# Kernel tuning notes

Measured on AMD Instinct MI355X. Metric: run time of the kernel, lower is better.

Reference implementation:

```python
import jax, jax.numpy as jnp
import numpy as np

NUM_EXPERTS = 32
TOP_K = 4
HIDDEN = 2048
INTER = 768


def setup_inputs() -> dict:
    key = jax.random.key(0)
    k1, k2, k3, k4 = jax.random.split(key, 4)
    hidden_states = jax.random.normal(k1, (4, 512, HIDDEN), dtype=jnp.float32)
    gate = jax.random.normal(k2, (HIDDEN, NUM_EXPERTS), dtype=jnp.float32) * 0.02
    gate_up_proj = jax.random.normal(k3, (NUM_EXPERTS, HIDDEN, 2 * INTER), dtype=jnp.float32) * 0.02
    down_proj = jax.random.normal(k4, (NUM_EXPERTS, INTER, HIDDEN), dtype=jnp.float32) * 0.02
    return {"hidden_states": hidden_states, "gate": gate,
            "gate_up_proj": gate_up_proj, "down_proj": down_proj}


def reference(hidden_states, gate, gate_up_proj, down_proj):
    batch_size = hidden_states.shape[0]
    x = hidden_states.reshape(-1, HIDDEN)  # (T, D)
    num_tokens = x.shape[0]

    # Router
    router_logits = jnp.einsum('TD,DE->TE', x, gate)
    routing_weights = jax.nn.softmax(router_logits.astype(jnp.float32), axis=-1)
    top_k_weights, top_k_indices = jax.lax.top_k(routing_weights, TOP_K)
    top_k_weights = top_k_weights / top_k_weights.sum(axis=-1, keepdims=True)
    top_k_weights = top_k_weights.astype(x.dtype)

    # Scatter top-k weights into full (T, E) matrix
    router_weights = jnp.zeros((num_tokens, NUM_EXPERTS), dtype=x.dtype)
    token_indices = jnp.broadcast_to(jnp.arange(num_tokens)[:, None], top_k_indices.shape)
    router_weights = router_weights.at[token_indices, top_k_indices].set(top_k_weights)

    # Dense all-expert experts pass (faithful to original: computes every expert per token)
    gate_up = jnp.einsum('TD,EDF->TEF', x, gate_up_proj)  # (T, E, 2F)
    g, u = jnp.split(gate_up, 2, axis=-1)
    gated = u * jax.nn.silu(g)  # (T, E, F)
    next_states = jnp.einsum('TEF,EFD->TED', gated, down_proj)
    next_states = (next_states * router_weights[..., None]).sum(axis=1)  # (T, D)
    return next_states.reshape(batch_size, -1, HIDDEN)
```

## Files before the change

### kernel.cpp

```cpp
#include <hip/hip_runtime.h>

#define T_TOKENS 2048
#define HIDDEN   2048
#define NEXPERT  32
#define TOPK     4
#define INTER    768
#define NPAIRS   (T_TOKENS*TOPK)
#define BM       128
#define BK       32
#define MT_MAX   95
#define NT1      12
#define NT2      16

typedef short  bh8 __attribute__((ext_vector_type(8)));
typedef float  fx4 __attribute__((ext_vector_type(4)));
typedef unsigned short us4 __attribute__((ext_vector_type(4)));

__device__ __forceinline__ unsigned short f2bf(float f){
    unsigned int u = __float_as_uint(f);
    u += 0x7FFFu + ((u >> 16) & 1u);
    return (unsigned short)(u >> 16);
}
__device__ __forceinline__ bh8 pk8(float4 a, float4 b){
    bh8 r;
    r[0]=(short)f2bf(a.x); r[1]=(short)f2bf(a.y); r[2]=(short)f2bf(a.z); r[3]=(short)f2bf(a.w);
    r[4]=(short)f2bf(b.x); r[5]=(short)f2bf(b.y); r[6]=(short)f2bf(b.z); r[7]=(short)f2bf(b.w);
    return r;
}

__global__ void router_k(const float* __restrict__ x, const float* __restrict__ gate,
                         int* __restrict__ topk_id, float* __restrict__ topk_w,
                         int* __restrict__ counts){
    const int t = blockIdx.x;
    const int l = threadIdx.x;
    const float* xr = x + (size_t)t*HIDDEN;
    float acc[NEXPERT];
#pragma unroll
    for (int e=0;e<NEXPERT;e++) acc[e]=0.f;
    for (int d=l; d<HIDDEN; d+=64){
        float xv = xr[d];
        const float4* g4 = (const float4*)(gate + (size_t)d*NEXPERT);
#pragma unroll
        for (int i=0;i<8;i++){
            float4 g = g4[i];
            acc[i*4+0] += xv*g.x; acc[i*4+1] += xv*g.y;
            acc[i*4+2] += xv*g.z; acc[i*4+3] += xv*g.w;
        }
    }
#pragma unroll
    for (int e=0;e<NEXPERT;e++){
#pragma unroll
        for (int m=1;m<64;m<<=1) acc[e] += __shfl_xor(acc[e], m, 64);
    }
    int ids[TOPK]; float lv[TOPK];
#pragma unroll
    for (int k=0;k<TOPK;k++){
        float m=-1e30f; int mi=0;
#pragma unroll
        for (int e=0;e<NEXPERT;e++){ if (acc[e]>m){ m=acc[e]; mi=e; } }
        ids[k]=mi; lv[k]=m; acc[mi]=-1e30f;
    }
    float ex[TOPK]; float s=0.f;
#pragma unroll
    for (int k=0;k<TOPK;k++){ ex[k]=__expf(lv[k]-lv[0]); s+=ex[k]; }
    if (l==0){
        float inv = 1.f/s;
#pragma unroll
        for (int k=0;k<TOPK;k++){
            topk_id[t*TOPK+k]=ids[k];
            topk_w[t*TOPK+k]=ex[k]*inv;
            atomicAdd(&counts[ids[k]],1);
        }
    }
}

__global__ void sched_k(const int* __restrict__ counts, int* __restrict__ offs,
                        int* __restrict__ cursors, int* __restrict__ nmt,
                        int* __restrict__ te, int* __restrict__ tr0, int* __restrict__ trn){
    if (threadIdx.x==0 && blockIdx.x==0){
        int tot=0, nm=0;
        for (int e=0;e<NEXPERT;e++){
            int c = counts[e];
            offs[e]=tot; cursors[e]=tot;
            for (int s=0;s<c;s+=BM){
                te[nm]=e; tr0[nm]=tot+s; trn[nm]=(c-s)<BM?(c-s):BM; nm++;
            }
            tot+=c;
        }
        *nmt = nm;
    }
}

__global__ void scatter_k(const int* __restrict__ topk_id, const float* __restrict__ topk_w,
                          int* __restrict__ cursors, int* __restrict__ pair_tok,
                          float* __restrict__ pair_w){
    int g = blockIdx.x*256 + threadIdx.x;
    int e = topk_id[g];
    float w = topk_w[g];
    int pos = atomicAdd(&cursors[e],1);
    pair_tok[pos] = g>>2;
    pair_w[pos]  = w;
}

__global__ __launch_bounds__(256) void gemm1_k(
        const float* __restrict__ x, const float* __restrict__ gup,
        const int* __restrict__ nmt, const int* __restrict__ te,
        const int* __restrict__ tr0, const int* __restrict__ trn,
        const int* __restrict__ pair_tok, const float* __restrict__ pair_w,
        unsigned short* __restrict__ gated){
    __shared__ unsigned short As[BM*40];
    __shared__ unsigned short Bs[BM*40];
    __shared__ int   s_tok[BM];
    __shared__ float s_w[BM];

    const int nwg = gridDim.x;
    const int q = nwg>>3, r = nwg&7;
    const int xcd = blockIdx.x & 7, idx = blockIdx.x >> 3;
    const int L = (xcd<r ? xcd*(q+1) : r*(q+1)+(xcd-r)*q) + idx;
    const int mt = L % MT_MAX, nt = L / MT_MAX;
    if (mt >= *nmt) return;
    const int e = te[mt], row0 = tr0[mt], rows = trn[mt];
    const int n0 = nt*64;

    const int t = threadIdx.x;
    if (t < BM){
        int p = row0 + t; if (p > NPAIRS-1) p = NPAIRS-1;
        s_tok[t] = pair_tok[p];
        s_w[t]   = pair_w[p];
    }
    __syncthreads();

    const int lane = t & 63, w = t >> 6;
    const int l15 = lane & 15, kb = lane >> 4;
    fx4 acc[2][8];
#pragma unroll
    for (int i=0;i<2;i++)
#pragma unroll
        for (int j=0;j<8;j++) acc[i][j] = (fx4)0.f;

    const float* bbase = gup + (size_t)e*HIDDEN*(2*INTER);
    const int ar = t>>1, akh = (t&1)*16;
    const int atok = s_tok[ar];
    const int bf0 = (t&31)*4, bd0 = (t>>5)*4;
    const int bch = bd0>>3, bhalf = ((bd0>>2)&1)*8;
    const int fc = (bf0 < 64) ? (n0 + bf0) : (768 + n0 + (bf0 - 64));

    for (int kt=0; kt<HIDDEN; kt+=BK){
        __syncthreads();
        {
            const float4* src = (const float4*)(x + (size_t)atok*HIDDEN + kt + akh);
            float4 v0=src[0], v1=src[1], v2=src[2], v3=src[3];
            bh8* dst = (bh8*)&As[ar*40 + akh];
            dst[0]=pk8(v0,v1); dst[1]=pk8(v2,v3);
        }
        {
            float4 rv0 = *(const float4*)(bbase + (size_t)(kt+bd0+0)*(2*INTER) + fc);
            float4 rv1 = *(const float4*)(bbase + (size_t)(kt+bd0+1)*(2*INTER) + fc);
            float4 rv2 = *(const float4*)(bbase + (size_t)(kt+bd0+2)*(2*INTER) + fc);
            float4 rv3 = *(const float4*)(bbase + (size_t)(kt+bd0+3)*(2*INTER) + fc);
            us4 c0 = { f2bf(rv0.x), f2bf(rv1.x), f2bf(rv2.x), f2bf(rv3.x) };
            us4 c1 = { f2bf(rv0.y), f2bf(rv1.y), f2bf(rv2.y), f2bf(rv3.y) };
            us4 c2 = { f2bf(rv0.z), f2bf(rv1.z), f2bf(rv2.z), f2bf(rv3.z) };
            us4 c3 = { f2bf(rv0.w), f2bf(rv1.w), f2bf(rv2.w), f2bf(rv3.w) };
            char* bsb = (char*)Bs;
            *(us4*)(bsb + (bf0+0)*80 + ((bch ^ 0)<<4) + bhalf) = c0;
            *(us4*)(bsb + (bf0+1)*80 + ((bch ^ 1)<<4) + bhalf) = c1;
            *(us4*)(bsb + (bf0+2)*80 + ((bch ^ 2)<<4) + bhalf) = c2;
            *(us4*)(bsb + (bf0+3)*80 + ((bch ^ 3)<<4) + bhalf) = c3;
        }
        __syncthreads();
        bh8 a0 = *(const bh8*)&As[(w*32 +      l15)*40 + kb*8];
        bh8 a1 = *(const bh8*)&As[(w*32 + 16 + l15)*40 + kb*8];
        const char* bsb = (const char*)Bs;
#pragma unroll
        for (int c=0;c<8;c++){
            bh8 b = *(const bh8*)(bsb + (c*16+l15)*80 + ((kb ^ (l15&3))<<4));
            acc[0][c] = __builtin_amdgcn_mfma_f32_16x16x32_bf16(a0, b, acc[0][c], 0,0,0);
            acc[1][c] = __builtin_amdgcn_mfma_f32_16x16x32_bf16(a1, b, acc[1][c], 0,0,0);
        }
    }

    const int rbase = w*32 + kb*4;
#pragma unroll
    for (int mr=0;mr<2;mr++){
#pragma unroll
        for (int qq=0;qq<4;qq++){
            int row = rbase + mr*16 + qq;
            if (row < rows){
                float wgt = s_w[row];
                size_t prow = (size_t)(row0 + row)*INTER + n0 + l15;
#pragma unroll
                for (int c=0;c<4;c++){
                    float g = acc[mr][c][qq], u = acc[mr][c+4][qq];
                    float sil = g / (1.f + __expf(-g));
                    gated[prow + c*16] = f2bf(sil*u*wgt);
                }
            }
        }
    }
}

__global__ __launch_bounds__(256) void gemm2_k(
        const unsigned short* __restrict__ gated, const float* __restrict__ down,
        const int* __restrict__ nmt, const int* __restrict__ te,
        const int* __restrict__ tr0, const int* __restrict__ trn,
        const int* __restrict__ pair_tok, float* __restrict__ out){
    __shared__ unsigned short As[BM*40];
    __shared__ unsigned short Bs[BM*40];
    __shared__ int s_tok[BM];

    const int nwg = gridDim.x;
    const int q = nwg>>3, r = nwg&7;
    const int xcd = blockIdx.x & 7, idx = blockIdx.x >> 3;
    const int L = (xcd<r ? xcd*(q+1) : r*(q+1)+(xcd-r)*q) + idx;
    const int mt = L % MT_MAX, nt = L / MT_MAX;
    if (mt >= *nmt) return;
    const int e = te[mt], row0 = tr0[mt], rows = trn[mt];
    const int n0 = nt*128;

    const int t = threadIdx.x;
    if (t < BM){
        int p = row0 + t; if (p > NPAIRS-1) p = NPAIRS-1;
        s_tok[t] = pair_tok[p];
    }
    __syncthreads();

    const int lane = t & 63, w = t >> 6;
    const int l15 = lane & 15, kb = lane >> 4;
    fx4 acc[2][8];
#pragma unroll
    for (int i=0;i<2;i++)
#pragma unroll
        for (int j=0;j<8;j++) acc[i][j] = (fx4)0.f;

    const float* bbase = down + (size_t)e*INTER*HIDDEN;
    const int ar = t>>1, akh = (t&1)*16;
    int ap = row0 + ar; if (ap > NPAIRS-1) ap = NPAIRS-1;
    const unsigned short* asrc = gated + (size_t)ap*INTER + akh;
    const int bf0 = (t&31)*4, bd0 = (t>>5)*4;
    const int bch = bd0>>3, bhalf = ((bd0>>2)&1)*8;
    const int fc = n0 + bf0;

    for (int kt=0; kt<INTER; kt+=BK){
        __syncthreads();
        {
            const bh8* s = (const bh8*)(asrc + kt);
            bh8 v0=s[0], v1=s[1];
            bh8* dst = (bh8*)&As[ar*40 + akh];
            dst[0]=v0; dst[1]=v1;
        }
        {
            float4 rv0 = *(const float4*)(bbase + (size_t)(kt+bd0+0)*HIDDEN + fc);
            float4 rv1 = *(const float4*)(bbase + (size_t)(kt+bd0+1)*HIDDEN + fc);
            float4 rv2 = *(const float4*)(bbase + (size_t)(kt+bd0+2)*HIDDEN + fc);
            float4 rv3 = *(const float4*)(bbase + (size_t)(kt+bd0+3)*HIDDEN + fc);
            us4 c0 = { f2bf(rv0.x), f2bf(rv1.x), f2bf(rv2.x), f2bf(rv3.x) };
            us4 c1 = { f2bf(rv0.y), f2bf(rv1.y), f2bf(rv2.y), f2bf(rv3.y) };
            us4 c2 = { f2bf(rv0.z), f2bf(rv1.z), f2bf(rv2.z), f2bf(rv3.z) };
            us4 c3 = { f2bf(rv0.w), f2bf(rv1.w), f2bf(rv2.w), f2bf(rv3.w) };
            char* bsb = (char*)Bs;
            *(us4*)(bsb + (bf0+0)*80 + ((bch ^ 0)<<4) + bhalf) = c0;
            *(us4*)(bsb + (bf0+1)*80 + ((bch ^ 1)<<4) + bhalf) = c1;
            *(us4*)(bsb + (bf0+2)*80 + ((bch ^ 2)<<4) + bhalf) = c2;
            *(us4*)(bsb + (bf0+3)*80 + ((bch ^ 3)<<4) + bhalf) = c3;
        }
        __syncthreads();
        bh8 a0 = *(const bh8*)&As[(w*32 +      l15)*40 + kb*8];
        bh8 a1 = *(const bh8*)&As[(w*32 + 16 + l15)*40 + kb*8];
        const char* bsb = (const char*)Bs;
#pragma unroll
        for (int c=0;c<8;c++){
            bh8 b = *(const bh8*)(bsb + (c*16+l15)*80 + ((kb ^ (l15&3))<<4));
            acc[0][c] = __builtin_amdgcn_mfma_f32_16x16x32_bf16(a0, b, acc[0][c], 0,0,0);
            acc[1][c] = __builtin_amdgcn_mfma_f32_16x16x32_bf16(a1, b, acc[1][c], 0,0,0);
        }
    }

    const int rbase = w*32 + kb*4;
#pragma unroll
    for (int mr=0;mr<2;mr++){
#pragma unroll
        for (int qq=0;qq<4;qq++){
            int row = rbase + mr*16 + qq;
            if (row < rows){
                float* orow = out + (size_t)s_tok[row]*HIDDEN + n0 + l15;
#pragma unroll
                for (int c=0;c<8;c++)
                    atomicAdd(orow + c*16, acc[mr][c][qq]);
            }
        }
    }
}

extern "C" void kernel_launch(void* const* d_in, const int* in_sizes, int n_in,
                              void* d_out, int out_size, void* d_ws, size_t ws_size,
                              hipStream_t stream){
    const float* x    = (const float*)d_in[0];
    const float* gate = (const float*)d_in[1];
    const float* gup  = (const float*)d_in[2];
    const float* down = (const float*)d_in[3];
    float* out = (float*)d_out;
    char*  ws  = (char*)d_ws;

    int*   topk_id  = (int*)  (ws + 0x00000);
    float* topk_w   = (float*)(ws + 0x08000);
    int*   counts   = (int*)  (ws + 0x10000);
    int*   cursors  = (int*)  (ws + 0x10080);
    int*   offs     = (int*)  (ws + 0x10100);
    int*   nmt      = (int*)  (ws + 0x10180);
    int*   te       = (int*)  (ws + 0x10200);
    int*   tr0      = (int*)  (ws + 0x10400);
    int*   trn      = (int*)  (ws + 0x10600);
    int*   pair_tok = (int*)  (ws + 0x10800);
    float* pair_w   = (float*)(ws + 0x18800);
    unsigned short* gated = (unsigned short*)(ws + 0x21000);

    hipMemsetAsync(d_out, 0, (size_t)out_size*sizeof(float), stream);
    hipMemsetAsync(counts, 0, NEXPERT*sizeof(int), stream);

    router_k <<<T_TOKENS, 64, 0, stream>>>(x, gate, topk_id, topk_w, counts);
    sched_k  <<<1, 64, 0, stream>>>(counts, offs, cursors, nmt, te, tr0, trn);
    scatter_k<<<NPAIRS/256, 256, 0, stream>>>(topk_id, topk_w, cursors, pair_tok, pair_w);
    gemm1_k  <<<MT_MAX*NT1, 256, 0, stream>>>(x, gup, nmt, te, tr0, trn, pair_tok, pair_w, gated);
    gemm2_k  <<<MT_MAX*NT2, 256, 0, stream>>>(gated, down, nmt, te, tr0, trn, pair_tok, out);
}
```

Measured before the change: 509.0 us.

## Prefetch next K tile via async global-to-LDS loads with double-buffered A

```diff
diff --git a/kernel.cpp b/kernel.cpp
--- a/kernel.cpp
+++ b/kernel.cpp
@@ -11,21 +11,39 @@
 #define MT_MAX   95
 #define NT1      12
 #define NT2      16
+#define NK1      (HIDDEN/BK)
+#define NK2      (INTER/BK)
 
 typedef short  bh8 __attribute__((ext_vector_type(8)));
 typedef float  fx4 __attribute__((ext_vector_type(4)));
-typedef unsigned short us4 __attribute__((ext_vector_type(4)));
-
-__device__ __forceinline__ unsigned short f2bf(float f){
-    unsigned int u = __float_as_uint(f);
-    u += 0x7FFFu + ((u >> 16) & 1u);
-    return (unsigned short)(u >> 16);
-}
-__device__ __forceinline__ bh8 pk8(float4 a, float4 b){
-    bh8 r;
-    r[0]=(short)f2bf(a.x); r[1]=(short)f2bf(a.y); r[2]=(short)f2bf(a.z); r[3]=(short)f2bf(a.w);
-    r[4]=(short)f2bf(b.x); r[5]=(short)f2bf(b.y); r[6]=(short)f2bf(b.z); r[7]=(short)f2bf(b.w);
-    return r;
+
+#define AS1 __attribute__((address_space(1)))
+#define AS3 __attribute__((address_space(3)))
+
+__device__ __forceinline__ void gload_lds16(const void* g, const void* lds_generic){
+    __builtin_amdgcn_global_load_lds(
+        (const AS1 void*)(unsigned long long)g,
+        (AS3 void*)(unsigned int)(unsigned long long)lds_generic,
+        16, 0, 0);
+}
+
+__device__ __forceinline__ unsigned int pack2bf(float a, float b){
+    unsigned ua = __float_as_uint(a) + 0x8000u;
+    unsigned ub = __float_as_uint(b) + 0x8000u;
+    return __builtin_amdgcn_perm(ub, ua, 0x07060302u);
+}
+__device__ __forceinline__ unsigned short f2bfu(float f){
+    return (unsigned short)((__float_as_uint(f) + 0x8000u) >> 16);
+}
+
+__global__ void cvt_x_k(const float* __restrict__ x, unsigned short* __restrict__ xb){
+    int i = (blockIdx.x*256 + threadIdx.x)*8;
+    float4 a = *(const float4*)(x+i);
+    float4 b = *(const float4*)(x+i+4);
+    uint4 o;
+    o.x = pack2bf(a.x,a.y); o.y = pack2bf(a.z,a.w);
+    o.z = pack2bf(b.x,b.y); o.w = pack2bf(b.z,b.w);
+    *(uint4*)(xb+i) = o;
 }
 
 __global__ void router_k(const float* __restrict__ x, const float* __restrict__ gate,
@@ -103,20 +121,20 @@
 }
 
 __global__ __launch_bounds__(256) void gemm1_k(
-        const float* __restrict__ x, const float* __restrict__ gup,
+        const unsigned short* __restrict__ xb, const float* __restrict__ gup,
         const int* __restrict__ nmt, const int* __restrict__ te,
         const int* __restrict__ tr0, const int* __restrict__ trn,
         const int* __restrict__ pair_tok, const float* __restrict__ pair_w,
         unsigned short* __restrict__ gated){
-    __shared__ unsigned short As[BM*40];
-    __shared__ unsigned short Bs[BM*40];
+    __shared__ __align__(16) unsigned short As[2][BM*32];
+    __shared__ __align__(16) unsigned short Bs[BM*40];
     __shared__ int   s_tok[BM];
     __shared__ float s_w[BM];
 
     const int nwg = gridDim.x;
     const int q = nwg>>3, r = nwg&7;
-    const int xcd = blockIdx.x & 7, idx = blockIdx.x >> 3;
-    const int L = (xcd<r ? xcd*(q+1) : r*(q+1)+(xcd-r)*q) + idx;
+    const int xcd = blockIdx.x & 7, bidx = blockIdx.x >> 3;
+    const int L = (xcd<r ? xcd*(q+1) : r*(q+1)+(xcd-r)*q) + bidx;
     const int mt = L % MT_MAX, nt = L / MT_MAX;
     if (mt >= *nmt) return;
     const int e = te[mt], row0 = tr0[mt], rows = trn[mt];
@@ -130,51 +148,62 @@
     }
     __syncthreads();
 
-    const int lane = t & 63, w = t >> 6;
+    const int w = t>>6, lane = t&63;
     const int l15 = lane & 15, kb = lane >> 4;
+
+    const int arow0 = w*16 + (lane>>2);
+    const int arow1 = 64 + arow0;
+    const int ck0 = (lane&3) ^ ((lane>>3)&3);
+    const unsigned short* asrc0 = xb + (size_t)s_tok[arow0]*HIDDEN + ck0*8;
+    const unsigned short* asrc1 = xb + (size_t)s_tok[arow1]*HIDDEN + ck0*8;
+    const unsigned short* adst0[2] = { &As[0][(w*16)*32],      &As[1][(w*16)*32] };
+    const unsigned short* adst1[2] = { &As[0][(64+w*16)*32],   &As[1][(64+w*16)*32] };
+
+    const int j5 = t & 31, col4 = j5*4;
+    const int bd0 = (t>>5)*4;
+    const int gq = (j5>>1)&3;
+    const unsigned wb = (unsigned)(col4*80 + (((bd0>>3) ^ gq)<<4) + (bd0&4)*2);
+    const int fc = (col4 < 64) ? (n0 + col4) : (704 + n0 + col4);
+    const float* bsrc = gup + (size_t)e*HIDDEN*(2*INTER) + (size_t)bd0*(2*INTER) + fc;
+
     fx4 acc[2][8];
 #pragma unroll
     for (int i=0;i<2;i++)
 #pragma unroll
         for (int j=0;j<8;j++) acc[i][j] = (fx4)0.f;
 
-    const float* bbase = gup + (size_t)e*HIDDEN*(2*INTER);
-    const int ar = t>>1, akh = (t&1)*16;
-    const int atok = s_tok[ar];
-    const int bf0 = (t&31)*4, bd0 = (t>>5)*4;
-    const int bch = bd0>>3, bhalf = ((bd0>>2)&1)*8;
-    const int fc = (bf0 < 64) ? (n0 + bf0) : (768 + n0 + (bf0 - 64));
-
-    for (int kt=0; kt<HIDDEN; kt+=BK){
+    gload_lds16(asrc0, adst0[0]);
+    gload_lds16(asrc1, adst1[0]);
+    float4 rv0 = *(const float4*)(bsrc);
+    float4 rv1 = *(const float4*)(bsrc + 2*INTER);
+    float4 rv2 = *(const float4*)(bsrc + 4*INTER);
+    float4 rv3 = *(const float4*)(bsrc + 6*INTER);
+
+    const int sA = (l15>>1)&3;
+    char* bsb = (char*)Bs;
+    for (int k=0; k<NK1; ++k){
         __syncthreads();
-        {
-            const float4* src = (const float4*)(x + (size_t)atok*HIDDEN + kt + akh);
-            float4 v0=src[0], v1=src[1], v2=src[2], v3=src[3];
-            bh8* dst = (bh8*)&As[ar*40 + akh];
-            dst[0]=pk8(v0,v1); dst[1]=pk8(v2,v3);
-        }
-        {
-            float4 rv0 = *(const float4*)(bbase + (size_t)(kt+bd0+0)*(2*INTER) + fc);
-            float4 rv1 = *(const float4*)(bbase + (size_t)(kt+bd0+1)*(2*INTER) + fc);
-            float4 rv2 = *(const float4*)(bbase + (size_t)(kt+bd0+2)*(2*INTER) + fc);
-            float4 rv3 = *(const float4*)(bbase + (size_t)(kt+bd0+3)*(2*INTER) + fc);
-            us4 c0 = { f2bf(rv0.x), f2bf(rv1.x), f2bf(rv2.x), f2bf(rv3.x) };
-            us4 c1 = { f2bf(rv0.y), f2bf(rv1.y), f2bf(rv2.y), f2bf(rv3.y) };
-            us4 c2 = { f2bf(rv0.z), f2bf(rv1.z), f2bf(rv2.z), f2bf(rv3.z) };
-            us4 c3 = { f2bf(rv0.w), f2bf(rv1.w), f2bf(rv2.w), f2bf(rv3.w) };
-            char* bsb = (char*)Bs;
-            *(us4*)(bsb + (bf0+0)*80 + ((bch ^ 0)<<4) + bhalf) = c0;
-            *(us4*)(bsb + (bf0+1)*80 + ((bch ^ 1)<<4) + bhalf) = c1;
-            *(us4*)(bsb + (bf0+2)*80 + ((bch ^ 2)<<4) + bhalf) = c2;
-            *(us4*)(bsb + (bf0+3)*80 + ((bch ^ 3)<<4) + bhalf) = c3;
-        }
+        *(uint2*)(bsb + wb      ) = make_uint2(pack2bf(rv0.x,rv1.x), pack2bf(rv2.x,rv3.x));
+        *(uint2*)(bsb + wb +  80) = make_uint2(pack2bf(rv0.y,rv1.y), pack2bf(rv2.y,rv3.y));
+        *(uint2*)(bsb + wb + 160) = make_uint2(pack2bf(rv0.z,rv1.z), pack2bf(rv2.z,rv3.z));
+        *(uint2*)(bsb + wb + 240) = make_uint2(pack2bf(rv0.w,rv1.w), pack2bf(rv2.w,rv3.w));
         __syncthreads();
-        bh8 a0 = *(const bh8*)&As[(w*32 +      l15)*40 + kb*8];
-        bh8 a1 = *(const bh8*)&As[(w*32 + 16 + l15)*40 + kb*8];
-        const char* bsb = (const char*)Bs;
+        if (k+1 < NK1){
+            const float* b2 = bsrc + (size_t)(k+1)*BK*(2*INTER);
+            rv0 = *(const float4*)(b2);
+            rv1 = *(const float4*)(b2 + 2*INTER);
+            rv2 = *(const float4*)(b2 + 4*INTER);
+            rv3 = *(const float4*)(b2 + 6*INTER);
+            gload_lds16(asrc0 + (k+1)*BK, adst0[(k+1)&1]);
+            gload_lds16(asrc1 + (k+1)*BK, adst1[(k+1)&1]);
+        }
+        const unsigned short* Ak = As[k&1];
+        bh8 a0 = *(const bh8*)(Ak + (w*32+l15)*32    + ((kb ^ sA)<<3));
+        bh8 a1 = *(const bh8*)(Ak + (w*32+16+l15)*32 + ((kb ^ sA)<<3));
 #pragma unroll
         for (int c=0;c<8;c++){
-            bh8 b = *(const bh8*)(bsb + (c*16+l15)*80 + ((kb ^ (l15&3))<<4));
+            const int bc = c*16 + l15;
+            bh8 b = *(const bh8*)(bsb + bc*80 + ((kb ^ ((bc>>3)&3))<<4));
             acc[0][c] = __builtin_amdgcn_mfma_f32_16x16x32_bf16(a0, b, acc[0][c], 0,0,0);
             acc[1][c] = __builtin_amdgcn_mfma_f32_16x16x32_bf16(a1, b, acc[1][c], 0,0,0);
         }
@@ -193,7 +222,7 @@
                 for (int c=0;c<4;c++){
                     float g = acc[mr][c][qq], u = acc[mr][c+4][qq];
                     float sil = g / (1.f + __expf(-g));
-                    gated[prow + c*16] = f2bf(sil*u*wgt);
+                    gated[prow + c*16] = f2bfu(sil*u*wgt);
                 }
             }
         }
@@ -205,14 +234,14 @@
         const int* __restrict__ nmt, const int* __restrict__ te,
         const int* __restrict__ tr0, const int* __restrict__ trn,
         const int* __restrict__ pair_tok, float* __restrict__ out){
-    __shared__ unsigned short As[BM*40];
-    __shared__ unsigned short Bs[BM*40];
+    __shared__ __align__(16) unsigned short As[2][BM*32];
+    __shared__ __align__(16) unsigned short Bs[BM*40];
     __shared__ int s_tok[BM];
 
     const int nwg = gridDim.x;
     const int q = nwg>>3, r = nwg&7;
-    const int xcd = blockIdx.x & 7, idx = blockIdx.x >> 3;
-    const int L = (xcd<r ? xcd*(q+1) : r*(q+1)+(xcd-r)*q) + idx;
+    const int xcd = blockIdx.x & 7, bidx = blockIdx.x >> 3;
+    const int L = (xcd<r ? xcd*(q+1) : r*(q+1)+(xcd-r)*q) + bidx;
     const int mt = L % MT_MAX, nt = L / MT_MAX;
     if (mt >= *nmt) return;
     const int e = te[mt], row0 = tr0[mt], rows = trn[mt];
@@ -225,52 +254,61 @@
     }
     __syncthreads();
 
-    const int lane = t & 63, w = t >> 6;
+    const int w = t>>6, lane = t&63;
     const int l15 = lane & 15, kb = lane >> 4;
+
+    const int arow0 = w*16 + (lane>>2);
+    const int arow1 = 64 + arow0;
+    const int ck0 = (lane&3) ^ ((lane>>3)&3);
+    const unsigned short* asrc0 = gated + (size_t)(row0 + arow0)*INTER + ck0*8;
+    const unsigned short* asrc1 = gated + (size_t)(row0 + arow1)*INTER + ck0*8;
+    const unsigned short* adst0[2] = { &As[0][(w*16)*32],    &As[1][(w*16)*32] };
+    const unsigned short* adst1[2] = { &As[0][(64+w*16)*32], &As[1][(64+w*16)*32] };
+
+    const int j5 = t & 31, col4 = j5*4;
+    const int bd0 = (t>>5)*4;
+    const int gq = (j5>>1)&3;
+    const unsigned wb = (unsigned)(col4*80 + (((bd0>>3) ^ gq)<<4) + (bd0&4)*2);
+    const float* bsrc = down + (size_t)e*INTER*HIDDEN + (size_t)bd0*HIDDEN + (n0 + col4);
+
     fx4 acc[2][8];
 #pragma unroll
     for (int i=0;i<2;i++)
 #pragma unroll
         for (int j=0;j<8;j++) acc[i][j] = (fx4)0.f;
 
-    const float* bbase = down + (size_t)e*INTER*HIDDEN;
-    const int ar = t>>1, akh = (t&1)*16;
-    int ap = row0 + ar; if (ap > NPAIRS-1) ap = NPAIRS-1;
-    const unsigned short* asrc = gated + (size_t)ap*INTER + akh;
-    const int bf0 = (t&31)*4, bd0 = (t>>5)*4;
-    const int bch = bd0>>3, bhalf = ((bd0>>2)&1)*8;
-    const int fc = n0 + bf0;
-
-    for (int kt=0; kt<INTER; kt+=BK){
+    gload_lds16(asrc0, adst0[0]);
+    gload_lds16(asrc1, adst1[0]);
+    float4 rv0 = *(const float4*)(bsrc);
+    float4 rv1 = *(const float4*)(bsrc + HIDDEN);
+    float4 rv2 = *(const float4*)(bsrc + 2*HIDDEN);
+    float4 rv3 = *(const float4*)(bsrc + 3*HIDDEN);
+
+    const int sA = (l15>>1)&3;
+    char* bsb = (char*)Bs;
+    for (int k=0; k<NK2; ++k){
         __syncthreads();
-        {
-            const bh8* s = (const bh8*)(asrc + kt);
-            bh8 v0=s[0], v1=s[1];
-            bh8* dst = (bh8*)&As[ar*40 + akh];
-            dst[0]=v0; dst[1]=v1;
-        }
-        {
-            float4 rv0 = *(const float4*)(bbase + (size_t)(kt+bd0+0)*HIDDEN + fc);
-            float4 rv1 = *(const float4*)(bbase + (size_t)(kt+bd0+1)*HIDDEN + fc);
-            float4 rv2 = *(const float4*)(bbase + (size_t)(kt+bd0+2)*HIDDEN + fc);
-            float4 rv3 = *(const float4*)(bbase + (size_t)(kt+bd0+3)*HIDDEN + fc);
-            us4 c0 = { f2bf(rv0.x), f2bf(rv1.x), f2bf(rv2.x), f2bf(rv3.x) };
-            us4 c1 = { f2bf(rv0.y), f2bf(rv1.y), f2bf(rv2.y), f2bf(rv3.y) };
-            us4 c2 = { f2bf(rv0.z), f2bf(rv1.z), f2bf(rv2.z), f2bf(rv3.z) };
-            us4 c3 = { f2bf(rv0.w), f2bf(rv1.w), f2bf(rv2.w), f2bf(rv3.w) };
-            char* bsb = (char*)Bs;
-            *(us4*)(bsb + (bf0+0)*80 + ((bch ^ 0)<<4) + bhalf) = c0;
-            *(us4*)(bsb + (bf0+1)*80 + ((bch ^ 1)<<4) + bhalf) = c1;
-            *(us4*)(bsb + (bf0+2)*80 + ((bch ^ 2)<<4) + bhalf) = c2;
-            *(us4*)(bsb + (bf0+3)*80 + ((bch ^ 3)<<4) + bhalf) = c3;
-        }
+        *(uint2*)(bsb + wb      ) = make_uint2(pack2bf(rv0.x,rv1.x), pack2bf(rv2.x,rv3.x));
+        *(uint2*)(bsb + wb +  80) = make_uint2(pack2bf(rv0.y,rv1.y), pack2bf(rv2.y,rv3.y));
+        *(uint2*)(bsb + wb + 160) = make_uint2(pack2bf(rv0.z,rv1.z), pack2bf(rv2.z,rv3.z));
+        *(uint2*)(bsb + wb + 240) = make_uint2(pack2bf(rv0.w,rv1.w), pack2bf(rv2.w,rv3.w));
         __syncthreads();
-        bh8 a0 = *(const bh8*)&As[(w*32 +      l15)*40 + kb*8];
-        bh8 a1 = *(const bh8*)&As[(w*32 + 16 + l15)*40 + kb*8];
-        const char* bsb = (const char*)Bs;
+        if (k+1 < NK2){
+            const float* b2 = bsrc + (size_t)(k+1)*BK*HIDDEN;
+            rv0 = *(const float4*)(b2);
+            rv1 = *(const float4*)(b2 + HIDDEN);
+            rv2 = *(const float4*)(b2 + 2*HIDDEN);
+            rv3 = *(const float4*)(b2 + 3*HIDDEN);
+            gload_lds16(asrc0 + (k+1)*BK, adst0[(k+1)&1]);
+            gload_lds16(asrc1 + (k+1)*BK, adst1[(k+1)&1]);
+        }
+        const unsigned short* Ak = As[k&1];
+        bh8 a0 = *(const bh8*)(Ak + (w*32+l15)*32    + ((kb ^ sA)<<3));
+        bh8 a1 = *(const bh8*)(Ak + (w*32+16+l15)*32 + ((kb ^ sA)<<3));
 #pragma unroll
         for (int c=0;c<8;c++){
-            bh8 b = *(const bh8*)(bsb + (c*16+l15)*80 + ((kb ^ (l15&3))<<4));
+            const int bc = c*16 + l15;
+            bh8 b = *(const bh8*)(bsb + bc*80 + ((kb ^ ((bc>>3)&3))<<4));
             acc[0][c] = __builtin_amdgcn_mfma_f32_16x16x32_bf16(a0, b, acc[0][c], 0,0,0);
             acc[1][c] = __builtin_amdgcn_mfma_f32_16x16x32_bf16(a1, b, acc[1][c], 0,0,0);
         }
@@ -314,13 +352,15 @@
     int*   pair_tok = (int*)  (ws + 0x10800);
     float* pair_w   = (float*)(ws + 0x18800);
     unsigned short* gated = (unsigned short*)(ws + 0x21000);
+    unsigned short* xb    = (unsigned short*)(ws + 0xC60000);
 
     hipMemsetAsync(d_out, 0, (size_t)out_size*sizeof(float), stream);
     hipMemsetAsync(counts, 0, NEXPERT*sizeof(int), stream);
 
+    cvt_x_k  <<<T_TOKENS*HIDDEN/(256*8), 256, 0, stream>>>(x, xb);
     router_k <<<T_TOKENS, 64, 0, stream>>>(x, gate, topk_id, topk_w, counts);
     sched_k  <<<1, 64, 0, stream>>>(counts, offs, cursors, nmt, te, tr0, trn);
     scatter_k<<<NPAIRS/256, 256, 0, stream>>>(topk_id, topk_w, cursors, pair_tok, pair_w);
-    gemm1_k  <<<MT_MAX*NT1, 256, 0, stream>>>(x, gup, nmt, te, tr0, trn, pair_tok, pair_w, gated);
+    gemm1_k  <<<MT_MAX*NT1, 256, 0, stream>>>(xb, gup, nmt, te, tr0, trn, pair_tok, pair_w, gated);
     gemm2_k  <<<MT_MAX*NT2, 256, 0, stream>>>(gated, down, nmt, te, tr0, trn, pair_tok, out);
 }
```

After: 429.0 us. 1.19x faster.
